# Performance work log

Measured on AMD Instinct MI355X. Metric: run time of the kernel, lower is better.

Reference implementation:

```python
import jax, jax.numpy as jnp
import numpy as np

N = 50000
E = 800000
D_IN = 128
D_HID = 128
D_OUT = 128
EPS = 1e-5


def setup_inputs() -> dict:
    key = jax.random.key(0)
    ks = jax.random.split(key, 10)
    x = jax.random.normal(ks[0], (N, D_IN), dtype=jnp.float32)
    edge_index = jax.random.randint(ks[1], (2, E), 0, N, dtype=jnp.int64)
    def lin(k, fi, fo):
        return jax.random.normal(k, (fi, fo), dtype=jnp.float32) / jnp.sqrt(jnp.float32(fi))
    return {
        "x": x,
        "edge_index": edge_index,
        "W1": lin(ks[2], D_IN, D_HID), "b1": jnp.zeros((D_HID,), jnp.float32),
        "W2": lin(ks[3], D_HID, D_HID), "b2": jnp.zeros((D_HID,), jnp.float32),
        "W3": lin(ks[4], D_HID, D_OUT), "b3": jnp.zeros((D_OUT,), jnp.float32),
        "g1": jnp.ones((D_HID,), jnp.float32), "be1": jnp.zeros((D_HID,), jnp.float32),
        "g2": jnp.ones((D_HID,), jnp.float32), "be2": jnp.zeros((D_HID,), jnp.float32),
    }


def _gcn_conv(x, src, dst, norm, W, b):
    # x' = D^{-1/2}(A+I)D^{-1/2} X W + b  (PyG GCNConv with self-loops)
    h = x @ W                              # [N, F]
    msgs = h[src] * norm[:, None]          # [E+N, F] gather
    agg = jax.ops.segment_sum(msgs, dst, num_segments=x.shape[0])  # scatter-add
    return agg + b


def _batchnorm(x, gamma, beta):
    mu = jnp.mean(x, axis=0)
    var = jnp.mean((x - mu) ** 2, axis=0)  # biased var, as in torch BN
    return (x - mu) * jax.lax.rsqrt(var + EPS) * gamma + beta


def reference(x, edge_index, W1, b1, W2, b2, W3, b3, g1, be1, g2, be2):
    n = x.shape[0]
    loops = jnp.arange(n, dtype=edge_index.dtype)
    src = jnp.concatenate([edge_index[0], loops])
    dst = jnp.concatenate([edge_index[1], loops])
    deg = jax.ops.segment_sum(jnp.ones_like(dst, dtype=x.dtype), dst, num_segments=n)
    dinv = jnp.where(deg > 0, jax.lax.rsqrt(deg), 0.0)
    norm = dinv[src] * dinv[dst]           # [E+N]

    h = _gcn_conv(x, src, dst, norm, W1, b1)
    h = jax.nn.relu(_batchnorm(h, g1, be1))
    h = _gcn_conv(h, src, dst, norm, W2, b2)
    h = jax.nn.relu(_batchnorm(h, g2, be2))
    h = _gcn_conv(h, src, dst, norm, W3, b3)
    # F.normalize(p=2, dim=-1)
    return h / jnp.maximum(jnp.linalg.norm(h, axis=-1, keepdims=True), 1e-12)
```

## Files before the change

### kernel.cpp

```cpp
#include <hip/hip_runtime.h>
#include <hip/hip_bf16.h>

#define D 128

typedef __bf16 bf16x8 __attribute__((ext_vector_type(8)));
typedef float floatx4 __attribute__((ext_vector_type(4)));


__global__ void k_count(const int* __restrict__ dst, int E, int* __restrict__ cnt) {
    int e = blockIdx.x * blockDim.x + threadIdx.x;
    if (e < E) atomicAdd(&cnt[dst[e]], 1);
}

__global__ __launch_bounds__(256) void k_scan1(const int* __restrict__ cnt, int n,
                                               int* __restrict__ bsum) {
    int i = blockIdx.x * 256 + threadIdx.x;
    int x = (i < n) ? cnt[i] : 0;
    #pragma unroll
    for (int off = 32; off > 0; off >>= 1) x += __shfl_xor(x, off, 64);
    __shared__ int ws[4];
    if ((threadIdx.x & 63) == 0) ws[threadIdx.x >> 6] = x;
    __syncthreads();
    if (threadIdx.x == 0) bsum[blockIdx.x] = ws[0] + ws[1] + ws[2] + ws[3];
}

__global__ void k_scan2(const int* __restrict__ bsum, int nb, int* __restrict__ boff) {
    int t = threadIdx.x;
    int lane = t & 63, wid = t >> 6;
    int x = (t < nb) ? bsum[t] : 0;
    int incl = x;
    #pragma unroll
    for (int off = 1; off < 64; off <<= 1) {
        int y = __shfl_up(incl, off, 64);
        if (lane >= off) incl += y;
    }
    __shared__ int ws[4];
    if (lane == 63) ws[wid] = incl;
    __syncthreads();
    int o = 0;
    for (int w = 0; w < wid; w++) o += ws[w];
    if (t < nb) boff[t] = o + incl - x;
}

__global__ __launch_bounds__(256) void k_scan3(const int* __restrict__ cnt,
                                               const int* __restrict__ boff, int n, int E,
                                               int* __restrict__ row_ptr, int* __restrict__ cursor,
                                               float* __restrict__ dinv) {
    int t = threadIdx.x;
    int lane = t & 63, wid = t >> 6;
    int i = blockIdx.x * 256 + t;
    int x = (i < n) ? cnt[i] : 0;
    int incl = x;
    #pragma unroll
    for (int off = 1; off < 64; off <<= 1) {
        int y = __shfl_up(incl, off, 64);
        if (lane >= off) incl += y;
    }
    __shared__ int ws[4];
    if (lane == 63) ws[wid] = incl;
    __syncthreads();
    int o = boff[blockIdx.x];
    for (int w = 0; w < wid; w++) o += ws[w];
    if (i < n) {
        int excl = o + incl - x;
        row_ptr[i] = excl;
        cursor[i] = excl;
        dinv[i] = rsqrtf((float)(x + 1));
    }
    if (blockIdx.x == 0 && t == 0) row_ptr[n] = E;
}

__global__ __launch_bounds__(256) void k_fill(const int* __restrict__ src,
                                              const int* __restrict__ dst, int E,
                                              int* __restrict__ cursor,
                                              unsigned short* __restrict__ esrc, int n) {
    int rs = (n + 7) >> 3;
    int lo = blockIdx.y * rs, hi = lo + rs;
    int step = gridDim.x * 256;
    for (int e = blockIdx.x * 256 + threadIdx.x; e < E; e += step) {
        int d = dst[e];
        int s = src[e];
        if (d >= lo && d < hi) {
            int p = atomicAdd(&cursor[d], 1);
            esrc[p] = (unsigned short)s;
        }
    }
}


__global__ __launch_bounds__(256) void k_prepw(const float* __restrict__ W1,
                                               const float* __restrict__ W2,
                                               const float* __restrict__ W3,
                                               unsigned short* __restrict__ Wt) {
    const float* W = (blockIdx.x == 0) ? W1 : (blockIdx.x == 1) ? W2 : W3;
    unsigned short* o = Wt + blockIdx.x * 16384;
    for (int i = threadIdx.x; i < 16384; i += 256) {
        int k = i >> 7, nn = i & 127;
        __hip_bfloat16 h = __float2bfloat16(W[i]);
        o[nn * 128 + k] = *(unsigned short*)&h;
    }
}


__global__ __launch_bounds__(256) void k_gemm(
    const float* __restrict__ X, const unsigned short* __restrict__ Wt,
    const float* __restrict__ scale, const float* __restrict__ stats_in,
    const float* __restrict__ gamma, const float* __restrict__ beta,
    float* __restrict__ stats_zero,
    unsigned* __restrict__ hs, int n, float invN) {
    __shared__ unsigned short Wl[128 * 128];
    __shared__ float bnl[256];
    int t = threadIdx.x;
    if (stats_in && t < 128) {
        float s = stats_in[t] + stats_in[256 + t] + stats_in[512 + t] + stats_in[768 + t];
        float q = stats_in[128 + t] + stats_in[384 + t] + stats_in[640 + t] + stats_in[896 + t];
        float mean = s * invN;
        float var = q * invN - mean * mean;
        float a = gamma[t] * rsqrtf(var + 1e-5f);
        bnl[t] = a;
        bnl[128 + t] = beta[t] - mean * a;
    }
    if (stats_zero && blockIdx.x == 0) {
        stats_zero[t] = 0.f;
        stats_zero[256 + t] = 0.f;
        stats_zero[512 + t] = 0.f;
        stats_zero[768 + t] = 0.f;
    }
    {
        const uint4* wg = (const uint4*)Wt;
        uint4* wl4 = (uint4*)Wl;
        #pragma unroll
        for (int j = 0; j < 8; j++) {
            int idx = j * 256 + t;
            int nn = idx >> 4, lc = idx & 15;
            wl4[nn * 16 + (lc ^ (nn & 15))] = wg[idx];
        }
    }
    __syncthreads();

    int l = t & 63, w = t >> 6;
    int lm = l & 15, quad = l >> 4;
    int m = blockIdx.x * 64 + w * 16 + lm;
    int rm = (m < n) ? m : (n - 1);
    const float* xrow = X + (size_t)rm * D;

    floatx4 acc[8];
    #pragma unroll
    for (int nt = 0; nt < 8; nt++) acc[nt] = (floatx4){0.f, 0.f, 0.f, 0.f};

    #pragma unroll
    for (int ks = 0; ks < 4; ks++) {
        int k0 = ks * 32 + quad * 8;
        float4 xa = *(const float4*)(xrow + k0);
        float4 xb = *(const float4*)(xrow + k0 + 4);
        if (stats_in) {
            float4 a0 = *(const float4*)&bnl[k0];
            float4 a1 = *(const float4*)&bnl[k0 + 4];
            float4 c0 = *(const float4*)&bnl[128 + k0];
            float4 c1 = *(const float4*)&bnl[128 + k0 + 4];
            xa.x = fmaxf(xa.x * a0.x + c0.x, 0.f);
            xa.y = fmaxf(xa.y * a0.y + c0.y, 0.f);
            xa.z = fmaxf(xa.z * a0.z + c0.z, 0.f);
            xa.w = fmaxf(xa.w * a0.w + c0.w, 0.f);
            xb.x = fmaxf(xb.x * a1.x + c1.x, 0.f);
            xb.y = fmaxf(xb.y * a1.y + c1.y, 0.f);
            xb.z = fmaxf(xb.z * a1.z + c1.z, 0.f);
            xb.w = fmaxf(xb.w * a1.w + c1.w, 0.f);
        }
        bf16x8 xf;
        xf[0] = (__bf16)xa.x; xf[1] = (__bf16)xa.y;
        xf[2] = (__bf16)xa.z; xf[3] = (__bf16)xa.w;
        xf[4] = (__bf16)xb.x; xf[5] = (__bf16)xb.y;
        xf[6] = (__bf16)xb.z; xf[7] = (__bf16)xb.w;
        int pc = (ks * 4 + quad) ^ lm;
        #pragma unroll
        for (int nt = 0; nt < 8; nt++) {
            const bf16x8 wf = *(const bf16x8*)&Wl[(nt * 16 + lm) * 128 + pc * 8];
            acc[nt] = __builtin_amdgcn_mfma_f32_16x16x32_bf16(wf, xf, acc[nt], 0, 0, 0);
        }
    }

    float s = scale[rm];
    if (m < n) {
        #pragma unroll
        for (int nt = 0; nt < 8; nt++) {
            __hip_bfloat16 h0 = __float2bfloat16(acc[nt][0] * s);
            __hip_bfloat16 h1 = __float2bfloat16(acc[nt][1] * s);
            __hip_bfloat16 h2 = __float2bfloat16(acc[nt][2] * s);
            __hip_bfloat16 h3 = __float2bfloat16(acc[nt][3] * s);
            uint2 uu;
            uu.x = (unsigned)*(unsigned short*)&h0 | ((unsigned)*(unsigned short*)&h1 << 16);
            uu.y = (unsigned)*(unsigned short*)&h2 | ((unsigned)*(unsigned short*)&h3 << 16);
            *(uint2*)&hs[((size_t)(nt >> 1) * n + m) * 16 + (nt & 1) * 8 + quad * 2] = uu;
        }
    }
}


__device__ inline float2 bf2f(unsigned u) {
    union { unsigned i; float f; } lo, hi;
    lo.i = u << 16;
    hi.i = u & 0xffff0000u;
    float2 r; r.x = lo.f; r.y = hi.f; return r;
}

__global__ __launch_bounds__(256) void k_agg(
    const unsigned* __restrict__ hs, const int* __restrict__ row_ptr,
    const unsigned short* __restrict__ esrc, const float* __restrict__ dinv,
    const float* __restrict__ bias, float* __restrict__ out,
    float* __restrict__ stats4, int n, int mode) {
    __shared__ float ls0[256], ls1[256], lq0[256], lq1[256];
    int t = threadIdx.x;
    int grp = t >> 4, sub = t & 15;
    int bid = blockIdx.x;
    int p = (bid >> 1) & 3;
    int nblk = (bid >> 3) * 2 + (bid & 1);
    int col32 = p * 16 + sub;
    const unsigned* hsp = hs + (size_t)p * n * 16;
    float s0 = 0.f, s1 = 0.f, q0 = 0.f, q1 = 0.f;
    int node0 = nblk * 64 + grp * 4;
    float2 b = *(const float2*)&bias[col32 * 2];

    for (int ni = 0; ni < 4; ni++) {
        int node = node0 + ni;
        if (node >= n) break;
        int beg = row_ptr[node], end = row_ptr[node + 1];
        float2 acc = bf2f(hsp[node * 16 + sub]);
        for (int base = beg; base < end; base += 16) {
            int m = end - base;
            if (m > 16) m = 16;
            int eid = (base + sub < end) ? (int)esrc[base + sub] : 0;
            int i = 0;
            for (; i + 8 <= m; i += 8) {
                int u0 = __shfl(eid, i + 0, 16);
                int u1 = __shfl(eid, i + 1, 16);
                int u2 = __shfl(eid, i + 2, 16);
                int u3 = __shfl(eid, i + 3, 16);
                int u4 = __shfl(eid, i + 4, 16);
                int u5 = __shfl(eid, i + 5, 16);
                int u6 = __shfl(eid, i + 6, 16);
                int u7 = __shfl(eid, i + 7, 16);
                unsigned p0 = hsp[u0 * 16 + sub];
                unsigned p1 = hsp[u1 * 16 + sub];
                unsigned p2 = hsp[u2 * 16 + sub];
                unsigned p3 = hsp[u3 * 16 + sub];
                unsigned p4 = hsp[u4 * 16 + sub];
                unsigned p5 = hsp[u5 * 16 + sub];
                unsigned p6 = hsp[u6 * 16 + sub];
                unsigned p7 = hsp[u7 * 16 + sub];
                float2 v0 = bf2f(p0), v1 = bf2f(p1), v2 = bf2f(p2), v3 = bf2f(p3);
                float2 v4 = bf2f(p4), v5 = bf2f(p5), v6 = bf2f(p6), v7 = bf2f(p7);
                acc.x += ((v0.x + v1.x) + (v2.x + v3.x)) + ((v4.x + v5.x) + (v6.x + v7.x));
                acc.y += ((v0.y + v1.y) + (v2.y + v3.y)) + ((v4.y + v5.y) + (v6.y + v7.y));
            }
            for (; i + 4 <= m; i += 4) {
                int u0 = __shfl(eid, i + 0, 16);
                int u1 = __shfl(eid, i + 1, 16);
                int u2 = __shfl(eid, i + 2, 16);
                int u3 = __shfl(eid, i + 3, 16);
                unsigned p0 = hsp[u0 * 16 + sub];
                unsigned p1 = hsp[u1 * 16 + sub];
                unsigned p2 = hsp[u2 * 16 + sub];
                unsigned p3 = hsp[u3 * 16 + sub];
                float2 v0 = bf2f(p0), v1 = bf2f(p1), v2 = bf2f(p2), v3 = bf2f(p3);
                acc.x += (v0.x + v1.x) + (v2.x + v3.x);
                acc.y += (v0.y + v1.y) + (v2.y + v3.y);
            }
            for (; i < m; i++) {
                int u = __shfl(eid, i, 16);
                float2 v = bf2f(hsp[u * 16 + sub]);
                acc.x += v.x;
                acc.y += v.y;
            }
        }
        float sc = dinv[node];
        float2 r;
        r.x = acc.x * sc + b.x;
        r.y = acc.y * sc + b.y;
        *(float2*)&out[(size_t)node * D + col32 * 2] = r;
        s0 += r.x; s1 += r.y;
        q0 += r.x * r.x; q1 += r.y * r.y;
    }

    if (mode == 0) {
        ls0[t] = s0; ls1[t] = s1; lq0[t] = q0; lq1[t] = q1;
        __syncthreads();
        if (t < 16) {
            float a0 = 0.f, a1 = 0.f, c0 = 0.f, c1 = 0.f;
            for (int g = 0; g < 16; g++) {
                int i = g * 16 + t;
                a0 += ls0[i]; a1 += ls1[i];
                c0 += lq0[i]; c1 += lq1[i];
            }
            float* sbuf = stats4 + ((bid >> 2) & 3) * 256;
            atomicAdd(&sbuf[p * 32 + 2 * t], a0);
            atomicAdd(&sbuf[p * 32 + 2 * t + 1], a1);
            atomicAdd(&sbuf[128 + p * 32 + 2 * t], c0);
            atomicAdd(&sbuf[128 + p * 32 + 2 * t + 1], c1);
        }
    }
}


__global__ __launch_bounds__(256) void k_l2norm(const float* __restrict__ h,
                                                float* __restrict__ out, int n) {
    int node = blockIdx.x * 4 + (threadIdx.x >> 6);
    if (node >= n) return;
    int lane = threadIdx.x & 63;
    float2 v = *(const float2*)&h[(size_t)node * D + lane * 2];
    float pw = v.x * v.x + v.y * v.y;
    #pragma unroll
    for (int off = 32; off > 0; off >>= 1) pw += __shfl_xor(pw, off, 64);
    float sc = 1.0f / fmaxf(sqrtf(pw), 1e-12f);
    float2 r;
    r.x = v.x * sc;
    r.y = v.y * sc;
    *(float2*)&out[(size_t)node * D + lane * 2] = r;
}


extern "C" void kernel_launch(void* const* d_in, const int* in_sizes, int n_in,
                              void* d_out, int out_size, void* d_ws, size_t ws_size,
                              hipStream_t stream) {
    const float* x  = (const float*)d_in[0];
    const int*   ei = (const int*)d_in[1];
    const float* W1 = (const float*)d_in[2];
    const float* b1 = (const float*)d_in[3];
    const float* W2 = (const float*)d_in[4];
    const float* b2 = (const float*)d_in[5];
    const float* W3 = (const float*)d_in[6];
    const float* b3 = (const float*)d_in[7];
    const float* g1 = (const float*)d_in[8];
    const float* be1 = (const float*)d_in[9];
    const float* g2 = (const float*)d_in[10];
    const float* be2 = (const float*)d_in[11];

    const int N = in_sizes[0] / D;
    const int E = in_sizes[1] / 2;
    const int* src = ei;
    const int* dst = ei + E;
    const float invN = 1.0f / (float)N;

    float* Y       = (float*)d_ws;
    unsigned short* hs = (unsigned short*)(Y + (size_t)N * D);
    float* dinv    = (float*)(hs + (size_t)N * D);
    float* statsA  = dinv + N;
    float* statsB  = statsA + 1024;
    unsigned short* wt = (unsigned short*)(statsB + 1024);
    int*   cnt     = (int*)(wt + 3 * 16384);
    int*   row_ptr = cnt + N;
    int*   cursor  = row_ptr + N + 1;
    int*   bsum    = cursor + N;
    int*   boff    = bsum + 256;
    unsigned short* esrc = (unsigned short*)(boff + 256);

    const int TB = 256;
    const int gE = (E + TB - 1) / TB;
    const int NB = (N + 255) / 256;
    const int gGemm = (N + 63) / 64;
    dim3 gFill(112, 8);
    const int gx = (N + 63) / 64;
    const int gxp = (gx + 1) & ~1;
    dim3 gAgg(gxp * 4);
    const int gNode = (N + 3) / 4;

    k_prepw<<<3, TB, 0, stream>>>(W1, W2, W3, wt);
    hipMemsetAsync(cnt, 0, (size_t)N * sizeof(int), stream);
    k_count<<<gE, TB, 0, stream>>>(dst, E, cnt);
    k_scan1<<<NB, TB, 0, stream>>>(cnt, N, bsum);
    k_scan2<<<1, 256, 0, stream>>>(bsum, NB, boff);
    k_scan3<<<NB, TB, 0, stream>>>(cnt, boff, N, E, row_ptr, cursor, dinv);
    k_fill<<<gFill, TB, 0, stream>>>(src, dst, E, cursor, esrc, N);

    k_gemm<<<gGemm, TB, 0, stream>>>(x, wt, dinv, nullptr, nullptr, nullptr, statsA,
                                     (unsigned*)hs, N, invN);
    k_agg<<<gAgg, TB, 0, stream>>>((const unsigned*)hs, row_ptr, esrc, dinv, b1, Y,
                                   statsA, N, 0);

    k_gemm<<<gGemm, TB, 0, stream>>>(Y, wt + 16384, dinv, statsA, g1, be1, statsB,
                                     (unsigned*)hs, N, invN);
    k_agg<<<gAgg, TB, 0, stream>>>((const unsigned*)hs, row_ptr, esrc, dinv, b2, Y,
                                   statsB, N, 0);

    k_gemm<<<gGemm, TB, 0, stream>>>(Y, wt + 32768, dinv, statsB, g2, be2, nullptr,
                                     (unsigned*)hs, N, invN);
    k_agg<<<gAgg, TB, 0, stream>>>((const unsigned*)hs, row_ptr, esrc, dinv, b3, Y,
                                   nullptr, N, 1);
    k_l2norm<<<gNode, TB, 0, stream>>>(Y, (float*)d_out, N);
}
```

Before: 368.0 us.

## Use persistent atomic work queue for aggregation with fixed-unroll gather loop

The aggregation kernel now launches a fixed grid of 2048 persistent blocks. Each block repeatedly grabs 32-node units from a per-column-slice atomic counter, which the preceding GEMM zeroes. The per-edge inner loop becomes a fully unrolled 16-wide masked FMA loop with the next chunk's edge indices prefetched, and each block handles two nodes per group instead of four. The aim is to balance irregular degree load and keep more gathers in flight, at the cost of redundant masked loads on short neighbor lists, extra barriers and atomics per unit, and a changed block-to-column mapping for the stats buffers.

```diff
diff --git a/kernel.cpp b/kernel.cpp
--- a/kernel.cpp
+++ b/kernel.cpp
@@ -106,7 +106,7 @@
     const float* __restrict__ X, const unsigned short* __restrict__ Wt,
     const float* __restrict__ scale, const float* __restrict__ stats_in,
     const float* __restrict__ gamma, const float* __restrict__ beta,
-    float* __restrict__ stats_zero,
+    float* __restrict__ stats_zero, int* __restrict__ wq,
     unsigned* __restrict__ hs, int n, float invN) {
     __shared__ unsigned short Wl[128 * 128];
     __shared__ float bnl[256];
@@ -120,11 +120,14 @@
         bnl[t] = a;
         bnl[128 + t] = beta[t] - mean * a;
     }
-    if (stats_zero && blockIdx.x == 0) {
-        stats_zero[t] = 0.f;
-        stats_zero[256 + t] = 0.f;
-        stats_zero[512 + t] = 0.f;
-        stats_zero[768 + t] = 0.f;
+    if (blockIdx.x == 0) {
+        if (stats_zero) {
+            stats_zero[t] = 0.f;
+            stats_zero[256 + t] = 0.f;
+            stats_zero[512 + t] = 0.f;
+            stats_zero[768 + t] = 0.f;
+        }
+        if (t < 8) wq[t] = 0;
     }
     {
         const uint4* wg = (const uint4*)Wt;
@@ -204,82 +207,75 @@
     float2 r; r.x = lo.f; r.y = hi.f; return r;
 }
 
+__device__ __forceinline__ void agg_node(
+    const unsigned* __restrict__ hsp, const unsigned short* __restrict__ esrc,
+    float* __restrict__ out, int node, int beg, int end, int eid,
+    unsigned selfv, float sc, float2 b, int sub, int col32,
+    float& s0, float& s1, float& q0, float& q1) {
+    float2 acc = bf2f(selfv);
+    for (int base = beg; base < end; base += 16) {
+        int m = end - base;
+        if (m > 16) m = 16;
+        int eidn = (base + 16 + sub < end) ? (int)esrc[base + 16 + sub] : 0;
+        #pragma unroll
+        for (int k = 0; k < 16; k++) {
+            int uk = __shfl(eid, (k < m) ? k : (m - 1), 16);
+            unsigned pv = hsp[(size_t)uk * 16 + sub];
+            float2 v = bf2f(pv);
+            float w = (k < m) ? 1.0f : 0.0f;
+            acc.x = fmaf(v.x, w, acc.x);
+            acc.y = fmaf(v.y, w, acc.y);
+        }
+        eid = eidn;
+    }
+    float2 r;
+    r.x = acc.x * sc + b.x;
+    r.y = acc.y * sc + b.y;
+    *(float2*)&out[(size_t)node * D + col32 * 2] = r;
+    s0 += r.x; s1 += r.y;
+    q0 += r.x * r.x; q1 += r.y * r.y;
+}
+
 __global__ __launch_bounds__(256) void k_agg(
     const unsigned* __restrict__ hs, const int* __restrict__ row_ptr,
     const unsigned short* __restrict__ esrc, const float* __restrict__ dinv,
     const float* __restrict__ bias, float* __restrict__ out,
-    float* __restrict__ stats4, int n, int mode) {
+    float* __restrict__ stats4, int* __restrict__ wq, int n, int nblks, int mode) {
     __shared__ float ls0[256], ls1[256], lq0[256], lq1[256];
+    __shared__ int snb;
     int t = threadIdx.x;
     int grp = t >> 4, sub = t & 15;
     int bid = blockIdx.x;
-    int p = (bid >> 1) & 3;
-    int nblk = (bid >> 3) * 2 + (bid & 1);
+    int p = (bid & 7) >> 1;
     int col32 = p * 16 + sub;
     const unsigned* hsp = hs + (size_t)p * n * 16;
     float s0 = 0.f, s1 = 0.f, q0 = 0.f, q1 = 0.f;
-    int node0 = nblk * 64 + grp * 4;
     float2 b = *(const float2*)&bias[col32 * 2];
 
-    for (int ni = 0; ni < 4; ni++) {
-        int node = node0 + ni;
-        if (node >= n) break;
-        int beg = row_ptr[node], end = row_ptr[node + 1];
-        float2 acc = bf2f(hsp[node * 16 + sub]);
-        for (int base = beg; base < end; base += 16) {
-            int m = end - base;
-            if (m > 16) m = 16;
-            int eid = (base + sub < end) ? (int)esrc[base + sub] : 0;
-            int i = 0;
-            for (; i + 8 <= m; i += 8) {
-                int u0 = __shfl(eid, i + 0, 16);
-                int u1 = __shfl(eid, i + 1, 16);
-                int u2 = __shfl(eid, i + 2, 16);
-                int u3 = __shfl(eid, i + 3, 16);
-                int u4 = __shfl(eid, i + 4, 16);
-                int u5 = __shfl(eid, i + 5, 16);
-                int u6 = __shfl(eid, i + 6, 16);
-                int u7 = __shfl(eid, i + 7, 16);
-                unsigned p0 = hsp[u0 * 16 + sub];
-                unsigned p1 = hsp[u1 * 16 + sub];
-                unsigned p2 = hsp[u2 * 16 + sub];
-                unsigned p3 = hsp[u3 * 16 + sub];
-                unsigned p4 = hsp[u4 * 16 + sub];
-                unsigned p5 = hsp[u5 * 16 + sub];
-                unsigned p6 = hsp[u6 * 16 + sub];
-                unsigned p7 = hsp[u7 * 16 + sub];
-                float2 v0 = bf2f(p0), v1 = bf2f(p1), v2 = bf2f(p2), v3 = bf2f(p3);
-                float2 v4 = bf2f(p4), v5 = bf2f(p5), v6 = bf2f(p6), v7 = bf2f(p7);
-                acc.x += ((v0.x + v1.x) + (v2.x + v3.x)) + ((v4.x + v5.x) + (v6.x + v7.x));
-                acc.y += ((v0.y + v1.y) + (v2.y + v3.y)) + ((v4.y + v5.y) + (v6.y + v7.y));
-            }
-            for (; i + 4 <= m; i += 4) {
-                int u0 = __shfl(eid, i + 0, 16);
-                int u1 = __shfl(eid, i + 1, 16);
-                int u2 = __shfl(eid, i + 2, 16);
-                int u3 = __shfl(eid, i + 3, 16);
-                unsigned p0 = hsp[u0 * 16 + sub];
-                unsigned p1 = hsp[u1 * 16 + sub];
-                unsigned p2 = hsp[u2 * 16 + sub];
-                unsigned p3 = hsp[u3 * 16 + sub];
-                float2 v0 = bf2f(p0), v1 = bf2f(p1), v2 = bf2f(p2), v3 = bf2f(p3);
-                acc.x += (v0.x + v1.x) + (v2.x + v3.x);
-                acc.y += (v0.y + v1.y) + (v2.y + v3.y);
-            }
-            for (; i < m; i++) {
-                int u = __shfl(eid, i, 16);
-                float2 v = bf2f(hsp[u * 16 + sub]);
-                acc.x += v.x;
-                acc.y += v.y;
-            }
-        }
-        float sc = dinv[node];
-        float2 r;
-        r.x = acc.x * sc + b.x;
-        r.y = acc.y * sc + b.y;
-        *(float2*)&out[(size_t)node * D + col32 * 2] = r;
-        s0 += r.x; s1 += r.y;
-        q0 += r.x * r.x; q1 += r.y * r.y;
+    for (;;) {
+        __syncthreads();
+        if (t == 0) snb = atomicAdd(&wq[p], 1);
+        __syncthreads();
+        int nblk = snb;
+        if (nblk >= nblks) break;
+        int node0 = nblk * 32 + grp * 2;
+        int i0 = node0 < n ? node0 : n;
+        int i1 = node0 + 1 < n ? node0 + 1 : n;
+        int i2 = node0 + 2 < n ? node0 + 2 : n;
+        int rp0 = row_ptr[i0], rp1 = row_ptr[i1], rp2 = row_ptr[i2];
+        int c0 = node0 < n ? node0 : n - 1;
+        int c1 = node0 + 1 < n ? node0 + 1 : n - 1;
+        unsigned sf0 = hsp[(size_t)c0 * 16 + sub];
+        unsigned sf1 = hsp[(size_t)c1 * 16 + sub];
+        float dv0 = dinv[c0], dv1 = dinv[c1];
+        int e0 = (rp0 + sub < rp1) ? (int)esrc[rp0 + sub] : 0;
+        int e1 = (rp1 + sub < rp2) ? (int)esrc[rp1 + sub] : 0;
+        if (node0 < n)
+            agg_node(hsp, esrc, out, node0, rp0, rp1, e0, sf0, dv0, b, sub, col32,
+                     s0, s1, q0, q1);
+        if (node0 + 1 < n)
+            agg_node(hsp, esrc, out, node0 + 1, rp1, rp2, e1, sf1, dv1, b, sub, col32,
+                     s0, s1, q0, q1);
     }
 
     if (mode == 0) {
@@ -352,16 +348,16 @@
     int*   cursor  = row_ptr + N + 1;
     int*   bsum    = cursor + N;
     int*   boff    = bsum + 256;
-    unsigned short* esrc = (unsigned short*)(boff + 256);
+    int*   wq      = boff + 256;
+    unsigned short* esrc = (unsigned short*)(wq + 8);
 
     const int TB = 256;
     const int gE = (E + TB - 1) / TB;
     const int NB = (N + 255) / 256;
     const int gGemm = (N + 63) / 64;
     dim3 gFill(112, 8);
-    const int gx = (N + 63) / 64;
-    const int gxp = (gx + 1) & ~1;
-    dim3 gAgg(gxp * 4);
+    const int gAgg = 2048;
+    const int aggUnits = (N + 31) / 32;
     const int gNode = (N + 3) / 4;
 
     k_prepw<<<3, TB, 0, stream>>>(W1, W2, W3, wt);
@@ -373,18 +369,18 @@
     k_fill<<<gFill, TB, 0, stream>>>(src, dst, E, cursor, esrc, N);
 
     k_gemm<<<gGemm, TB, 0, stream>>>(x, wt, dinv, nullptr, nullptr, nullptr, statsA,
-                                     (unsigned*)hs, N, invN);
+                                     wq, (unsigned*)hs, N, invN);
     k_agg<<<gAgg, TB, 0, stream>>>((const unsigned*)hs, row_ptr, esrc, dinv, b1, Y,
-                                   statsA, N, 0);
+                                   statsA, wq, N, aggUnits, 0);
 
     k_gemm<<<gGemm, TB, 0, stream>>>(Y, wt + 16384, dinv, statsA, g1, be1, statsB,
-                                     (unsigned*)hs, N, invN);
+                                     wq, (unsigned*)hs, N, invN);
     k_agg<<<gAgg, TB, 0, stream>>>((const unsigned*)hs, row_ptr, esrc, dinv, b2, Y,
-                                   statsB, N, 0);
+                                   statsB, wq, N, aggUnits, 0);
 
     k_gemm<<<gGemm, TB, 0, stream>>>(Y, wt + 32768, dinv, statsB, g2, be2, nullptr,
-                                     (unsigned*)hs, N, invN);
+                                     wq, (unsigned*)hs, N, invN);
     k_agg<<<gAgg, TB, 0, stream>>>((const unsigned*)hs, row_ptr, esrc, dinv, b3, Y,
-                                   nullptr, N, 1);
+                                   nullptr, wq, N, aggUnits, 1);
     k_l2norm<<<gNode, TB, 0, stream>>>(Y, (float*)d_out, N);
 }
```

New measurement: 540.5 us. 1.47x slower.

## Restructure aggregation gather into 16-byte loads with four edges per 16-lane group

Applied to the files above, without the earlier changes.

The aggregation kernel now has each 16-lane group split into 4 edge slots by 4 column quarters. Each lane issues 16-byte vector loads of 8 bf16 features, which replaces per-lane 4-byte loads with 8- and 4-way unrolled shuffles. Partial sums are reduced across the edge slots with xor shuffles. The kernel also preloads row pointers, prefetches the next chunk of edge indices, and accumulates BN statistics in shared memory instead of per-thread registers. The aim is fewer, wider memory transactions per edge. In exchange there is padded wasted work when degrees are not multiples of 4 and extra shuffle reduction cost.

```diff
diff --git a/kernel.cpp b/kernel.cpp
--- a/kernel.cpp
+++ b/kernel.cpp
@@ -209,94 +209,148 @@
     const unsigned short* __restrict__ esrc, const float* __restrict__ dinv,
     const float* __restrict__ bias, float* __restrict__ out,
     float* __restrict__ stats4, int n, int mode) {
-    __shared__ float ls0[256], ls1[256], lq0[256], lq1[256];
+    __shared__ float lsS[16][32];
+    __shared__ float lsQ[16][32];
     int t = threadIdx.x;
     int grp = t >> 4, sub = t & 15;
+    int qd = sub >> 2;
+    int qe = sub & 3;
     int bid = blockIdx.x;
     int p = (bid >> 1) & 3;
     int nblk = (bid >> 3) * 2 + (bid & 1);
-    int col32 = p * 16 + sub;
     const unsigned* hsp = hs + (size_t)p * n * 16;
-    float s0 = 0.f, s1 = 0.f, q0 = 0.f, q1 = 0.f;
+
+    lsS[t >> 5][t & 31] = 0.f;
+    lsS[(t >> 5) + 8][t & 31] = 0.f;
+    lsQ[t >> 5][t & 31] = 0.f;
+    lsQ[(t >> 5) + 8][t & 31] = 0.f;
+    __syncthreads();
+
+    float4 bA = *(const float4*)&bias[p * 32 + qe * 8];
+    float4 bB = *(const float4*)&bias[p * 32 + qe * 8 + 4];
+
     int node0 = nblk * 64 + grp * 4;
-    float2 b = *(const float2*)&bias[col32 * 2];
-
+    int rp[5];
+    #pragma unroll
+    for (int k = 0; k < 5; k++) {
+        int ik = node0 + k;
+        if (ik > n) ik = n;
+        rp[k] = row_ptr[ik];
+    }
+
+    #pragma unroll
     for (int ni = 0; ni < 4; ni++) {
         int node = node0 + ni;
         if (node >= n) break;
-        int beg = row_ptr[node], end = row_ptr[node + 1];
-        float2 acc = bf2f(hsp[node * 16 + sub]);
+        int beg = rp[ni], end = rp[ni + 1];
+        float sc = dinv[node];
+        int e_cur = (beg + sub < end) ? (int)esrc[beg + sub] : 0;
+        uint4 sv = *(const uint4*)&hsp[(size_t)node * 16 + qe * 4];
+        float2 a0 = bf2f(qd == 0 ? sv.x : 0u);
+        float2 a1 = bf2f(qd == 0 ? sv.y : 0u);
+        float2 a2 = bf2f(qd == 0 ? sv.z : 0u);
+        float2 a3 = bf2f(qd == 0 ? sv.w : 0u);
+
         for (int base = beg; base < end; base += 16) {
-            int m = end - base;
-            if (m > 16) m = 16;
-            int eid = (base + sub < end) ? (int)esrc[base + sub] : 0;
-            int i = 0;
-            for (; i + 8 <= m; i += 8) {
-                int u0 = __shfl(eid, i + 0, 16);
-                int u1 = __shfl(eid, i + 1, 16);
-                int u2 = __shfl(eid, i + 2, 16);
-                int u3 = __shfl(eid, i + 3, 16);
-                int u4 = __shfl(eid, i + 4, 16);
-                int u5 = __shfl(eid, i + 5, 16);
-                int u6 = __shfl(eid, i + 6, 16);
-                int u7 = __shfl(eid, i + 7, 16);
-                unsigned p0 = hsp[u0 * 16 + sub];
-                unsigned p1 = hsp[u1 * 16 + sub];
-                unsigned p2 = hsp[u2 * 16 + sub];
-                unsigned p3 = hsp[u3 * 16 + sub];
-                unsigned p4 = hsp[u4 * 16 + sub];
-                unsigned p5 = hsp[u5 * 16 + sub];
-                unsigned p6 = hsp[u6 * 16 + sub];
-                unsigned p7 = hsp[u7 * 16 + sub];
-                float2 v0 = bf2f(p0), v1 = bf2f(p1), v2 = bf2f(p2), v3 = bf2f(p3);
-                float2 v4 = bf2f(p4), v5 = bf2f(p5), v6 = bf2f(p6), v7 = bf2f(p7);
-                acc.x += ((v0.x + v1.x) + (v2.x + v3.x)) + ((v4.x + v5.x) + (v6.x + v7.x));
-                acc.y += ((v0.y + v1.y) + (v2.y + v3.y)) + ((v4.y + v5.y) + (v6.y + v7.y));
-            }
-            for (; i + 4 <= m; i += 4) {
-                int u0 = __shfl(eid, i + 0, 16);
-                int u1 = __shfl(eid, i + 1, 16);
-                int u2 = __shfl(eid, i + 2, 16);
-                int u3 = __shfl(eid, i + 3, 16);
-                unsigned p0 = hsp[u0 * 16 + sub];
-                unsigned p1 = hsp[u1 * 16 + sub];
-                unsigned p2 = hsp[u2 * 16 + sub];
-                unsigned p3 = hsp[u3 * 16 + sub];
-                float2 v0 = bf2f(p0), v1 = bf2f(p1), v2 = bf2f(p2), v3 = bf2f(p3);
-                acc.x += (v0.x + v1.x) + (v2.x + v3.x);
-                acc.y += (v0.y + v1.y) + (v2.y + v3.y);
-            }
-            for (; i < m; i++) {
-                int u = __shfl(eid, i, 16);
-                float2 v = bf2f(hsp[u * 16 + sub]);
-                acc.x += v.x;
-                acc.y += v.y;
-            }
-        }
-        float sc = dinv[node];
-        float2 r;
-        r.x = acc.x * sc + b.x;
-        r.y = acc.y * sc + b.y;
-        *(float2*)&out[(size_t)node * D + col32 * 2] = r;
-        s0 += r.x; s1 += r.y;
-        q0 += r.x * r.x; q1 += r.y * r.y;
+            int mm = end - base;
+            if (mm > 16) mm = 16;
+            int e_nxt = (base + 16 + sub < end) ? (int)esrc[base + 16 + sub] : 0;
+            int u0, u1, u2, u3;
+            float w0, w1, w2, w3;
+            {
+                int ei = qd;
+                int ix = ei < mm ? ei : mm - 1;
+                u0 = __shfl(e_cur, ix, 16);
+                w0 = ei < mm ? 1.f : 0.f;
+            }
+            {
+                int ei = 4 + qd;
+                int ix = ei < mm ? ei : mm - 1;
+                u1 = __shfl(e_cur, ix, 16);
+                w1 = ei < mm ? 1.f : 0.f;
+            }
+            {
+                int ei = 8 + qd;
+                int ix = ei < mm ? ei : mm - 1;
+                u2 = __shfl(e_cur, ix, 16);
+                w2 = ei < mm ? 1.f : 0.f;
+            }
+            {
+                int ei = 12 + qd;
+                int ix = ei < mm ? ei : mm - 1;
+                u3 = __shfl(e_cur, ix, 16);
+                w3 = ei < mm ? 1.f : 0.f;
+            }
+            uint4 g0 = *(const uint4*)&hsp[(size_t)u0 * 16 + qe * 4];
+            uint4 g1 = *(const uint4*)&hsp[(size_t)u1 * 16 + qe * 4];
+            uint4 g2 = *(const uint4*)&hsp[(size_t)u2 * 16 + qe * 4];
+            uint4 g3 = *(const uint4*)&hsp[(size_t)u3 * 16 + qe * 4];
+            float2 v;
+            v = bf2f(g0.x); a0.x = fmaf(v.x, w0, a0.x); a0.y = fmaf(v.y, w0, a0.y);
+            v = bf2f(g0.y); a1.x = fmaf(v.x, w0, a1.x); a1.y = fmaf(v.y, w0, a1.y);
+            v = bf2f(g0.z); a2.x = fmaf(v.x, w0, a2.x); a2.y = fmaf(v.y, w0, a2.y);
+            v = bf2f(g0.w); a3.x = fmaf(v.x, w0, a3.x); a3.y = fmaf(v.y, w0, a3.y);
+            v = bf2f(g1.x); a0.x = fmaf(v.x, w1, a0.x); a0.y = fmaf(v.y, w1, a0.y);
+            v = bf2f(g1.y); a1.x = fmaf(v.x, w1, a1.x); a1.y = fmaf(v.y, w1, a1.y);
+            v = bf2f(g1.z); a2.x = fmaf(v.x, w1, a2.x); a2.y = fmaf(v.y, w1, a2.y);
+            v = bf2f(g1.w); a3.x = fmaf(v.x, w1, a3.x); a3.y = fmaf(v.y, w1, a3.y);
+            v = bf2f(g2.x); a0.x = fmaf(v.x, w2, a0.x); a0.y = fmaf(v.y, w2, a0.y);
+            v = bf2f(g2.y); a1.x = fmaf(v.x, w2, a1.x); a1.y = fmaf(v.y, w2, a1.y);
+            v = bf2f(g2.z); a2.x = fmaf(v.x, w2, a2.x); a2.y = fmaf(v.y, w2, a2.y);
+            v = bf2f(g2.w); a3.x = fmaf(v.x, w2, a3.x); a3.y = fmaf(v.y, w2, a3.y);
+            v = bf2f(g3.x); a0.x = fmaf(v.x, w3, a0.x); a0.y = fmaf(v.y, w3, a0.y);
+            v = bf2f(g3.y); a1.x = fmaf(v.x, w3, a1.x); a1.y = fmaf(v.y, w3, a1.y);
+            v = bf2f(g3.z); a2.x = fmaf(v.x, w3, a2.x); a2.y = fmaf(v.y, w3, a2.y);
+            v = bf2f(g3.w); a3.x = fmaf(v.x, w3, a3.x); a3.y = fmaf(v.y, w3, a3.y);
+            e_cur = e_nxt;
+        }
+
+        a0.x += __shfl_xor(a0.x, 4, 16); a0.x += __shfl_xor(a0.x, 8, 16);
+        a0.y += __shfl_xor(a0.y, 4, 16); a0.y += __shfl_xor(a0.y, 8, 16);
+        a1.x += __shfl_xor(a1.x, 4, 16); a1.x += __shfl_xor(a1.x, 8, 16);
+        a1.y += __shfl_xor(a1.y, 4, 16); a1.y += __shfl_xor(a1.y, 8, 16);
+        a2.x += __shfl_xor(a2.x, 4, 16); a2.x += __shfl_xor(a2.x, 8, 16);
+        a2.y += __shfl_xor(a2.y, 4, 16); a2.y += __shfl_xor(a2.y, 8, 16);
+        a3.x += __shfl_xor(a3.x, 4, 16); a3.x += __shfl_xor(a3.x, 8, 16);
+        a3.y += __shfl_xor(a3.y, 4, 16); a3.y += __shfl_xor(a3.y, 8, 16);
+
+        if (qd == 0) {
+            float4 r0, r1;
+            r0.x = fmaf(a0.x, sc, bA.x);
+            r0.y = fmaf(a0.y, sc, bA.y);
+            r0.z = fmaf(a1.x, sc, bA.z);
+            r0.w = fmaf(a1.y, sc, bA.w);
+            r1.x = fmaf(a2.x, sc, bB.x);
+            r1.y = fmaf(a2.y, sc, bB.y);
+            r1.z = fmaf(a3.x, sc, bB.z);
+            r1.w = fmaf(a3.y, sc, bB.w);
+            float* op = &out[(size_t)node * D + p * 32 + qe * 8];
+            *(float4*)op = r0;
+            *(float4*)(op + 4) = r1;
+            if (mode == 0) {
+                lsS[grp][qe * 8 + 0] += r0.x; lsQ[grp][qe * 8 + 0] += r0.x * r0.x;
+                lsS[grp][qe * 8 + 1] += r0.y; lsQ[grp][qe * 8 + 1] += r0.y * r0.y;
+                lsS[grp][qe * 8 + 2] += r0.z; lsQ[grp][qe * 8 + 2] += r0.z * r0.z;
+                lsS[grp][qe * 8 + 3] += r0.w; lsQ[grp][qe * 8 + 3] += r0.w * r0.w;
+                lsS[grp][qe * 8 + 4] += r1.x; lsQ[grp][qe * 8 + 4] += r1.x * r1.x;
+                lsS[grp][qe * 8 + 5] += r1.y; lsQ[grp][qe * 8 + 5] += r1.y * r1.y;
+                lsS[grp][qe * 8 + 6] += r1.z; lsQ[grp][qe * 8 + 6] += r1.z * r1.z;
+                lsS[grp][qe * 8 + 7] += r1.w; lsQ[grp][qe * 8 + 7] += r1.w * r1.w;
+            }
+        }
     }
 
     if (mode == 0) {
-        ls0[t] = s0; ls1[t] = s1; lq0[t] = q0; lq1[t] = q1;
         __syncthreads();
-        if (t < 16) {
-            float a0 = 0.f, a1 = 0.f, c0 = 0.f, c1 = 0.f;
+        if (t < 32) {
+            float a = 0.f, c = 0.f;
             for (int g = 0; g < 16; g++) {
-                int i = g * 16 + t;
-                a0 += ls0[i]; a1 += ls1[i];
-                c0 += lq0[i]; c1 += lq1[i];
+                a += lsS[g][t];
+                c += lsQ[g][t];
             }
             float* sbuf = stats4 + ((bid >> 2) & 3) * 256;
-            atomicAdd(&sbuf[p * 32 + 2 * t], a0);
-            atomicAdd(&sbuf[p * 32 + 2 * t + 1], a1);
-            atomicAdd(&sbuf[128 + p * 32 + 2 * t], c0);
-            atomicAdd(&sbuf[128 + p * 32 + 2 * t + 1], c1);
+            atomicAdd(&sbuf[p * 32 + t], a);
+            atomicAdd(&sbuf[128 + p * 32 + t], c);
         }
     }
 }
```

After: 334.0 us. 1.1x faster.
